# Performance work log

Hardware: AMD Instinct MI355X
Metric: run time of the kernel (lower is better)

The kernel has to match this reference:

```python
import jax, jax.numpy as jnp
import numpy as np

H, D, DIM = 8, 128, 1024   # heads, dim_head, model dim (inner_dim = H*D = DIM)
QB, N = 16, 512            # 'q' and 'n' dims of the [q, n, dim] inputs


def layer_norm(x, g, b, eps=1e-5):
    mu = x.mean(-1, keepdims=True)
    var = ((x - mu) ** 2).mean(-1, keepdims=True)
    return (x - mu) / jnp.sqrt(var + eps) * g + b


def setup_inputs() -> dict:
    key = jax.random.key(0)
    ks = jax.random.split(key, 8)
    rn = lambda k, shape, s=1.0: jax.random.normal(k, shape, jnp.float32) * s
    return {
        'q': rn(ks[0], (QB, N, DIM)),
        'k': rn(ks[1], (QB, N, DIM)),
        'v': rn(ks[2], (QB, N, DIM)),
        'ln_g': jnp.ones(DIM, jnp.float32),
        'ln_b': jnp.zeros(DIM, jnp.float32),
        'w_in': rn(ks[3], (H * D, DIM), 0.02),          # Linear(dim -> inner_dim), no bias
        'wp_w1': rn(ks[4], (D, 2 * D), 0.05),           # weight_predictor Linear(2d -> d)
        'wp_b1': jnp.zeros(D, jnp.float32),
        'wp_ln_g': jnp.ones(D, jnp.float32),
        'wp_ln_b': jnp.zeros(D, jnp.float32),
        'wp_w2': rn(ks[5], (3, D), 0.05),               # Linear(d -> 3)
        'wp_b2': jnp.zeros(3, jnp.float32),
        'w_out': rn(ks[6], (DIM, H * D), 0.02),         # output Linear(inner_dim -> dim)
        'b_out': jnp.zeros(DIM, jnp.float32),
    }


def reference(q, k, v, ln_g, ln_b, w_in, wp_w1, wp_b1, wp_ln_g, wp_ln_b,
              wp_w2, wp_b2, w_out, b_out):
    def proj(t):
        x = layer_norm(t, ln_g, ln_b) @ w_in.T                 # [Q, N, H*D]
        Qd, Nd = t.shape[0], t.shape[1]
        return x.reshape(Qd, Nd, H, D).transpose(2, 0, 1, 3)   # [h, q, n, d]

    f_q, f_k, f_v = proj(q), proj(k), proj(v)

    # cosine similarity component
    dots = jnp.einsum('hqnd,hqmd->hqnm', f_q, f_k)
    qn = jnp.linalg.norm(f_q, axis=-1)                          # [h, q, n]
    kn = jnp.linalg.norm(f_k, axis=-1)                          # [h, q, m]
    cosine_sim = dots / (qn[..., :, None] * kn[..., None, :])

    q_centered = f_q - f_q.mean(-1, keepdims=True)

    # variance component (unbiased variance, clipped ratio vs target_var=1)
    q_var = jnp.var(f_q, axis=-1, ddof=1)
    k_var = jnp.var(f_k, axis=-1, ddof=1)
    q_ratio = 2.0 * jnp.minimum(q_var, 1.0) / (q_var + 1.0)
    k_ratio = 2.0 * jnp.minimum(k_var, 1.0) / (k_var + 1.0)
    var_component = jnp.einsum('hqn,hqm->hqnm', q_ratio, k_ratio)

    # decorrelation-scaled covariance component (overwrites the dead loop in the source)
    q_flat = q_centered.reshape(H, -1, D)                        # [h, q*n, d]
    feat_corr = jnp.einsum('hnd,hne->hde', q_flat, q_flat) / q_flat.shape[1]
    feat_corr = feat_corr * (1.0 - jnp.eye(D, dtype=feat_corr.dtype))
    decorr_score = jnp.linalg.norm(feat_corr, axis=(-2, -1)) / (D * D)
    decorr_scale = jnp.exp(-5.0 * decorr_score)[:, None, None, None]
    cov_component = cosine_sim * decorr_scale

    # dynamic per-head weight mixing
    q_global = f_q.mean(axis=(1, 2))                             # [h, d]
    k_global = f_k.mean(axis=(1, 2))
    feats = jnp.concatenate([q_global, k_global], axis=-1)       # [h, 2d]
    h1 = jnp.maximum(layer_norm(feats @ wp_w1.T + wp_b1, wp_ln_g, wp_ln_b), 0.0)
    weights = jax.nn.softmax(h1 @ wp_w2.T + wp_b2, axis=-1)      # [h, 3]
    cw = weights[:, 0][:, None, None, None]
    vw = weights[:, 1][:, None, None, None]
    ww = weights[:, 2][:, None, None, None]
    mixed = cw * cosine_sim + vw * cov_component + ww * var_component

    out = jnp.einsum('hqnm,hqmd->hqnd', mixed, f_v)
    out = out.transpose(1, 2, 0, 3).reshape(q.shape[0], q.shape[1], H * D)
    return out @ w_out.T + b_out
```

## Files before the change

kernel.cpp:

```cpp
#include <hip/hip_runtime.h>
#include <hip/hip_bf16.h>

typedef unsigned short u16;
typedef __attribute__((ext_vector_type(8))) short short8;
typedef __attribute__((ext_vector_type(4))) float floatx4;

#define H 8
#define D 128
#define DIM 1024
#define QB 16
#define NSEQ 512
#define R 8192

__device__ inline u16 f2b(float x) {
    union { float f; unsigned int u; } c{x};
    unsigned int lsb = (c.u >> 16) & 1;
    unsigned int r = c.u + 0x7fffu + lsb;
    return (u16)(r >> 16);
}
__device__ inline float b2f(u16 u) {
    union { unsigned int i; float f; } c;
    c.i = (unsigned int)u << 16;
    return c.f;
}

#define GLOAD_LDS16(gptr, lptr)                                                        \
    __builtin_amdgcn_global_load_lds(                                                  \
        (const __attribute__((address_space(1))) unsigned int*)(gptr),                 \
        (__attribute__((address_space(3))) unsigned int*)(lptr), 16, 0, 0)

__global__ __launch_bounds__(256) void prep(const float* __restrict__ q,
                                            const float* __restrict__ k,
                                            const float* __restrict__ v,
                                            const float* __restrict__ g,
                                            const float* __restrict__ b,
                                            u16* __restrict__ out,
                                            const float* __restrict__ w_in,
                                            const float* __restrict__ w_out,
                                            u16* __restrict__ w_in16,
                                            u16* __restrict__ w_out16) {
    const int bb = blockIdx.x;
    const int tid = threadIdx.x;
    if (bb < 2048) {
        const int n4each = DIM * DIM / 4;
        int i = bb * 256 + tid;
        const float* src; u16* dst; int j;
        if (i < n4each) { src = w_in;  dst = w_in16;  j = i; }
        else            { src = w_out; dst = w_out16; j = i - n4each; }
        float4 vv = *(const float4*)(src + (size_t)j * 4);
        ushort4 pk;
        pk.x = f2b(vv.x); pk.y = f2b(vv.y); pk.z = f2b(vv.z); pk.w = f2b(vv.w);
        *(ushort4*)(dst + (size_t)j * 4) = pk;
        return;
    }
    const int b2 = bb - 2048;
    const int y = b2 >> 13;
    const int r = b2 & 8191;
    const float* src = (y == 0) ? q : (y == 1) ? k : v;
    const int wv = tid >> 6, lane = tid & 63;
    const float* row = src + (size_t)r * DIM;
    float4 vv = *(const float4*)(row + tid * 4);
    float sum = vv.x + vv.y + vv.z + vv.w;
    float sq = vv.x * vv.x + vv.y * vv.y + vv.z * vv.z + vv.w * vv.w;
#pragma unroll
    for (int o = 32; o > 0; o >>= 1) {
        sum += __shfl_xor(sum, o);
        sq  += __shfl_xor(sq, o);
    }
    __shared__ float s1[4], s2[4];
    if (lane == 0) { s1[wv] = sum; s2[wv] = sq; }
    __syncthreads();
    sum = s1[0] + s1[1] + s1[2] + s1[3];
    sq  = s2[0] + s2[1] + s2[2] + s2[3];
    float mean = sum * (1.0f / DIM);
    float var = sq * (1.0f / DIM) - mean * mean;
    float rstd = rsqrtf(var + 1e-5f);
    float4 gv = *(const float4*)(g + tid * 4);
    float4 bv = *(const float4*)(b + tid * 4);
    ushort4 pk;
    pk.x = f2b((vv.x - mean) * rstd * gv.x + bv.x);
    pk.y = f2b((vv.y - mean) * rstd * gv.y + bv.y);
    pk.z = f2b((vv.z - mean) * rstd * gv.z + bv.z);
    pk.w = f2b((vv.w - mean) * rstd * gv.w + bv.w);
    *(ushort4*)(out + ((size_t)y * R + r) * DIM + tid * 4) = pk;
}

__global__ __launch_bounds__(256) void gemm_qkv(const u16* __restrict__ A,
                                                const u16* __restrict__ B,
                                                u16* __restrict__ qT,
                                                u16* __restrict__ fqb,
                                                u16* __restrict__ kTh,
                                                u16* __restrict__ vT,
                                                float* __restrict__ qn,
                                                float* __restrict__ qm,
                                                float* __restrict__ qr,
                                                float* __restrict__ kn,
                                                float* __restrict__ kr) {
    __shared__ __align__(16) u16 smem[19712];
    u16* As  = smem;
    u16* Bs  = smem + 4096;
    u16* As2 = smem + 8192;
    u16* Bs2 = smem + 12288;
    float* sred = (float*)(smem + 18432);
    float* invb = (float*)(smem + 19456);

    const int tid = threadIdx.x;
    const int bb = blockIdx.x;
    const int xcd = bb & 7, j0 = bb >> 3;
    const int h = j0 & 7;
    const int rowblk = xcd * 24 + (j0 >> 3);
    const int m0 = rowblk * 128, n0 = h * 128;
    const int seg = rowblk >> 6;
    const int lrb = (rowblk & 63) * 128;

    const int wave = tid >> 6, lane = tid & 63;
    const int wm = (wave >> 1) * 64, wn = (wave & 1) * 64;
    const int fr = lane & 15, kq = lane >> 4;
    const int srow = tid >> 2, scol = (tid & 3) * 8;

    floatx4 acc[4][4] = {};
    const size_t aOff0 = (size_t)(m0 + srow) * DIM + scol;
    const size_t aOff1 = (size_t)(m0 + 64 + srow) * DIM + scol;
    const size_t bOff0 = (size_t)(n0 + srow) * DIM + scol;
    const size_t bOff1 = (size_t)(n0 + 64 + srow) * DIM + scol;

    for (int kt = 0; kt < DIM; kt += 64) {
        GLOAD_LDS16(A + aOff0 + kt, As + tid * 8);
        GLOAD_LDS16(A + aOff1 + kt, As + (256 + tid) * 8);
        GLOAD_LDS16(B + bOff0 + kt, Bs + tid * 8);
        GLOAD_LDS16(B + bOff1 + kt, Bs + (256 + tid) * 8);
        GLOAD_LDS16(A + aOff0 + kt + 32, As2 + tid * 8);
        GLOAD_LDS16(A + aOff1 + kt + 32, As2 + (256 + tid) * 8);
        GLOAD_LDS16(B + bOff0 + kt + 32, Bs2 + tid * 8);
        GLOAD_LDS16(B + bOff1 + kt + 32, Bs2 + (256 + tid) * 8);
        __syncthreads();
        short8 xf[4], wf[4];
#pragma unroll
        for (int i = 0; i < 4; i++)
            xf[i] = *(const short8*)&As[(wm + i * 16 + fr) * 32 + kq * 8];
#pragma unroll
        for (int j = 0; j < 4; j++)
            wf[j] = *(const short8*)&Bs[(wn + j * 16 + fr) * 32 + kq * 8];
#pragma unroll
        for (int j = 0; j < 4; j++)
#pragma unroll
            for (int i = 0; i < 4; i++)
                acc[j][i] = __builtin_amdgcn_mfma_f32_16x16x32_bf16(wf[j], xf[i], acc[j][i], 0, 0, 0);
        short8 xg[4], wg[4];
#pragma unroll
        for (int i = 0; i < 4; i++)
            xg[i] = *(const short8*)&As2[(wm + i * 16 + fr) * 32 + kq * 8];
#pragma unroll
        for (int j = 0; j < 4; j++)
            wg[j] = *(const short8*)&Bs2[(wn + j * 16 + fr) * 32 + kq * 8];
#pragma unroll
        for (int j = 0; j < 4; j++)
#pragma unroll
            for (int i = 0; i < 4; i++)
                acc[j][i] = __builtin_amdgcn_mfma_f32_16x16x32_bf16(wg[j], xg[i], acc[j][i], 0, 0, 0);
        __syncthreads();
    }

    if (seg <= 1) {
        const int half = wn >> 6;
#pragma unroll
        for (int i = 0; i < 4; i++) {
            float s = 0.0f, qs = 0.0f;
#pragma unroll
            for (int j = 0; j < 4; j++)
#pragma unroll
                for (int rg = 0; rg < 4; rg++) {
                    float vv = acc[j][i][rg];
                    s += vv; qs += vv * vv;
                }
            s += __shfl_xor(s, 16); qs += __shfl_xor(qs, 16);
            s += __shfl_xor(s, 32); qs += __shfl_xor(qs, 32);
            if (kq == 0) {
                int rl = wm + i * 16 + fr;
                sred[rl * 4 + half * 2 + 0] = s;
                sred[rl * 4 + half * 2 + 1] = qs;
            }
        }
        __syncthreads();
        if (tid < 128) {
            float sum = sred[tid * 4 + 0] + sred[tid * 4 + 2];
            float sq  = sred[tid * 4 + 1] + sred[tid * 4 + 3];
            float nrm = sqrtf(sq);
            float var = (sq - sum * sum * (1.0f / D)) * (1.0f / (D - 1));
            float ratio = 2.0f * fminf(var, 1.0f) / (var + 1.0f);
            size_t idx = (size_t)h * R + lrb + tid;
            if (seg == 0) {
                qn[idx] = nrm; qm[idx] = sum * (1.0f / D); qr[idx] = ratio;
            } else {
                kn[idx] = nrm; kr[idx] = ratio;
                invb[tid] = 1.0f / nrm;
            }
        }
        __syncthreads();
    }

    u16* dstT = (seg == 0) ? qT : (seg == 1) ? kTh : vT;
#pragma unroll
    for (int i = 0; i < 4; i++) {
        const int rl = wm + i * 16 + fr;
        const float sc = (seg == 1) ? invb[rl] : 1.0f;
#pragma unroll
        for (int j = 0; j < 4; j++) {
#pragma unroll
            for (int rg = 0; rg < 4; rg++) {
                const int cl = wn + j * 16 + kq * 4 + rg;
                dstT[(size_t)(h * D + cl) * R + lrb + rl] = f2b(acc[j][i][rg] * sc);
            }
        }
    }

    if (seg == 0) {
        __syncthreads();
        u16* Tw = smem + wave * 4608;
#pragma unroll
        for (int i = 0; i < 4; i++)
#pragma unroll
            for (int j = 0; j < 4; j++) {
                ushort4 pk;
                pk.x = f2b(acc[j][i][0]); pk.y = f2b(acc[j][i][1]);
                pk.z = f2b(acc[j][i][2]); pk.w = f2b(acc[j][i][3]);
                *(ushort4*)&Tw[(i * 16 + fr) * 72 + j * 16 + kq * 4] = pk;
            }
        __syncthreads();
#pragma unroll
        for (int p = 0; p < 16; p++) {
            int rloc = p * 4 + kq;
            int c4 = fr * 4;
            ushort4 v = *(const ushort4*)&Tw[rloc * 72 + c4];
            *(ushort4*)&fqb[(size_t)(lrb + wm + rloc) * DIM + h * D + wn + c4] = v;
        }
    }
}

__global__ __launch_bounds__(256) void fanout(const u16* __restrict__ qT,
                                              const u16* __restrict__ kTh,
                                              const u16* __restrict__ vT,
                                              const float* __restrict__ qm,
                                              const float* __restrict__ kn,
                                              const float* __restrict__ kr,
                                              float* __restrict__ qg,
                                              float* __restrict__ kg,
                                              float* __restrict__ ubuf,
                                              float* __restrict__ s2,
                                              float* __restrict__ P,
                                              u16* __restrict__ Mt,
                                              float* __restrict__ sv) {
    __shared__ __align__(16) u16 sm[8832];
    u16* As = sm;
    u16* Bs = sm + 4096;
    float* wbuf  = (float*)(sm + 8192);
    float* svred = (float*)(sm + 8256);
    float* redS  = (float*)(sm + 8768);

    const int bb = blockIdx.x;
    const int tid = threadIdx.x;
    const int wave = tid >> 6, lane = tid & 63;
    const int wm = (wave >> 1) * 64, wn = (wave & 1) * 64;
    const int fr = lane & 15, kq = lane >> 4;
    const int srow = tid >> 2, scol = (tid & 3) * 8;

    if (bb < 128) {
        const int qi = bb & 15, h = bb >> 4;
        const int m0g = qi * 512;
        const size_t a0 = (size_t)(h * D + srow) * R + m0g + scol;
        const size_t a1 = (size_t)(h * D + 64 + srow) * R + m0g + scol;
        const int e_id = tid & 127, mb16 = (tid >> 7) * 16;
        float svacc = 0.0f;
        floatx4 acc[4][4] = {};
        for (int kt = 0; kt < 512; kt += 32) {
            GLOAD_LDS16(vT + a0 + kt, As + tid * 8);
            GLOAD_LDS16(vT + a1 + kt, As + (256 + tid) * 8);
            GLOAD_LDS16(kTh + a0 + kt, Bs + tid * 8);
            GLOAD_LDS16(kTh + a1 + kt, Bs + (256 + tid) * 8);
            if (tid < 32) wbuf[tid] = kr[(size_t)h * R + m0g + kt + tid];
            __syncthreads();
            short8 af[4], bf[4];
#pragma unroll
            for (int i = 0; i < 4; i++)
                af[i] = *(const short8*)&As[(wm + i * 16 + fr) * 32 + kq * 8];
#pragma unroll
            for (int j = 0; j < 4; j++)
                bf[j] = *(const short8*)&Bs[(wn + j * 16 + fr) * 32 + kq * 8];
#pragma unroll
            for (int i = 0; i < 4; i++)
#pragma unroll
                for (int j = 0; j < 4; j++)
                    acc[i][j] = __builtin_amdgcn_mfma_f32_16x16x32_bf16(af[i], bf[j], acc[i][j], 0, 0, 0);
            {
                short8 va = *(const short8*)&As[e_id * 32 + mb16];
                short8 vb = *(const short8*)&As[e_id * 32 + mb16 + 8];
#pragma unroll
                for (int jm = 0; jm < 8; jm++)
                    svacc += b2f((u16)va[jm]) * wbuf[mb16 + jm];
#pragma unroll
                for (int jm = 0; jm < 8; jm++)
                    svacc += b2f((u16)vb[jm]) * wbuf[mb16 + 8 + jm];
            }
            __syncthreads();
        }
        u16* mb = Mt + (size_t)(h * QB + qi) * D * D;
#pragma unroll
        for (int i = 0; i < 4; i++) {
            int er = wm + i * 16 + kq * 4;
#pragma unroll
            for (int j = 0; j < 4; j++) {
                int dc = wn + j * 16 + fr;
#pragma unroll
                for (int r = 0; r < 4; r++)
                    mb[(size_t)(er + r) * D + dc] = f2b(acc[i][j][r]);
            }
        }
        svred[tid] = svacc;
        __syncthreads();
        if (tid < 128)
            sv[(size_t)(h * QB + qi) * D + tid] = svred[tid] + svred[tid + 128];
    } else if (bb < 192) {
        const int t = bb - 128;
        const int c = t & 7, h = t >> 3;
        floatx4 acc[4][4] = {};
        const size_t a0 = (size_t)(h * D + srow) * R + c * 1024 + scol;
        const size_t a1 = (size_t)(h * D + 64 + srow) * R + c * 1024 + scol;
        for (int kt = 0; kt < 1024; kt += 32) {
            GLOAD_LDS16(qT + a0 + kt, As + tid * 8);
            GLOAD_LDS16(qT + a1 + kt, As + (256 + tid) * 8);
            __syncthreads();
            short8 af[4], bf[4];
#pragma unroll
            for (int i = 0; i < 4; i++)
                af[i] = *(const short8*)&As[(wm + i * 16 + fr) * 32 + kq * 8];
#pragma unroll
            for (int j = 0; j < 4; j++)
                bf[j] = *(const short8*)&As[(wn + j * 16 + fr) * 32 + kq * 8];
#pragma unroll
            for (int i = 0; i < 4; i++)
#pragma unroll
                for (int j = 0; j < 4; j++)
                    acc[i][j] = __builtin_amdgcn_mfma_f32_16x16x32_bf16(af[i], bf[j], acc[i][j], 0, 0, 0);
            __syncthreads();
        }
        float* base = P + (size_t)(h * 8 + c) * (D * D);
#pragma unroll
        for (int i = 0; i < 4; i++) {
            int dr = wm + i * 16 + kq * 4;
#pragma unroll
            for (int j = 0; j < 4; j++) {
                int ec = wn + j * 16 + fr;
                float4 f4;
                f4.x = acc[i][j][0]; f4.y = acc[i][j][1];
                f4.z = acc[i][j][2]; f4.w = acc[i][j][3];
                *(float4*)&base[(size_t)ec * D + dr] = f4;
            }
        }
    } else {
        const int t = bb - 192;
        const int dg = t & 15, h = (t >> 4) & 7, mode = t >> 7;
        const u16* fT = mode ? kTh : qT;
        const float* wvec = mode ? kn : qm;
        const int wv = tid >> 6;
        float (*red)[4] = (float(*)[4])redS;
        const float* wp = wvec + (size_t)h * R;
        for (int dd = 0; dd < 8; dd++) {
            int d = dg * 8 + dd;
            const u16* rowp = fT + (size_t)(h * D + d) * R;
            float s = 0.0f, su = 0.0f;
            for (int it = 0; it < 8; it++) {
                int r = it * 1024 + tid * 4;
                uint2 pv = *(const uint2*)(rowp + r);
                float4 w = *(const float4*)(wp + r);
                float v0 = b2f((u16)(pv.x & 0xffffu)), v1 = b2f((u16)(pv.x >> 16));
                float v2 = b2f((u16)(pv.y & 0xffffu)), v3 = b2f((u16)(pv.y >> 16));
                if (mode) s += v0 * w.x + v1 * w.y + v2 * w.z + v3 * w.w;
                else {
                    s += v0 + v1 + v2 + v3;
                    su += v0 * w.x + v1 * w.y + v2 * w.z + v3 * w.w;
                }
            }
#pragma unroll
            for (int o = 32; o > 0; o >>= 1) {
                s += __shfl_xor(s, o);
                su += __shfl_xor(su, o);
            }
            if ((tid & 63) == 0) { red[0][wv] = s; red[1][wv] = su; }
            __syncthreads();
            if (tid == 0) {
                float S  = red[0][0] + red[0][1] + red[0][2] + red[0][3];
                float SU = red[1][0] + red[1][1] + red[1][2] + red[1][3];
                if (mode) kg[h * D + d] = S * (1.0f / R);
                else { qg[h * D + d] = S * (1.0f / R); ubuf[h * D + d] = SU; }
            }
            __syncthreads();
        }
        if (!mode && dg == 0) {
            float tt = 0.0f;
            for (int it = 0; it < 8; it++) {
                float4 m4 = *(const float4*)(qm + (size_t)h * R + it * 1024 + tid * 4);
                tt += m4.x * m4.x + m4.y * m4.y + m4.z * m4.z + m4.w * m4.w;
            }
#pragma unroll
            for (int o = 32; o > 0; o >>= 1) tt += __shfl_xor(tt, o);
            if ((tid & 63) == 0) red[0][wv] = tt;
            __syncthreads();
            if (tid == 0) s2[h] = red[0][0] + red[0][1] + red[0][2] + red[0][3];
        }
    }
}

__global__ __launch_bounds__(256) void decorr_sum(const float* __restrict__ P,
                                                  const float* __restrict__ ubuf,
                                                  const float* __restrict__ s2b,
                                                  float* __restrict__ Spart) {
    int bx = blockIdx.x, h = blockIdx.y, tid = threadIdx.x;
    float s2h = s2b[h];
    float S = 0.0f;
    for (int t = 0; t < 2; t++) {
        int de = bx * 512 + t * 256 + tid;
        int dd = de >> 7, ee = de & 127;
        float g = 0.0f;
        for (int c = 0; c < 8; c++)
            g += P[(size_t)(h * 8 + c) * (D * D) + de];
        if (dd != ee) {
            float vv = (g - ubuf[h * D + dd] - ubuf[h * D + ee] + s2h) * (1.0f / R);
            S += vv * vv;
        }
    }
#pragma unroll
    for (int o = 32; o > 0; o >>= 1) S += __shfl_xor(S, o);
    __shared__ float r1[4];
    if ((tid & 63) == 0) r1[tid >> 6] = S;
    __syncthreads();
    if (tid == 0) Spart[h * 32 + bx] = r1[0] + r1[1] + r1[2] + r1[3];
}

__global__ __launch_bounds__(256) void head_kernel(const float* __restrict__ Spart,
                                                   const float* __restrict__ qg,
                                                   const float* __restrict__ kg,
                                                   const float* __restrict__ w1,
                                                   const float* __restrict__ b1,
                                                   const float* __restrict__ lng,
                                                   const float* __restrict__ lnb,
                                                   const float* __restrict__ w2,
                                                   const float* __restrict__ b2,
                                                   float* __restrict__ coef) {
    int h = blockIdx.x, tid = threadIdx.x;
    __shared__ float s1[256], s2[256], s3[256];
    __shared__ float feats[256];
    float Ssum = 0.0f;
    for (int c = 0; c < 32; c++) Ssum += Spart[h * 32 + c];
    float dscale = expf(-5.0f * sqrtf(Ssum) / (float)(D * D));
    feats[tid] = (tid < 128) ? qg[h * D + tid] : kg[h * D + tid - 128];
    __syncthreads();
    float yv = 0.0f;
    if (tid < 128) {
        float a = b1[tid];
        for (int i = 0; i < 256; i++) a = fmaf(feats[i], w1[tid * 256 + i], a);
        yv = a;
    }
    s1[tid] = (tid < 128) ? yv : 0.0f;
    s2[tid] = (tid < 128) ? yv * yv : 0.0f;
    __syncthreads();
    for (int s = 128; s > 0; s >>= 1) {
        if (tid < s) { s1[tid] += s1[tid + s]; s2[tid] += s2[tid + s]; }
        __syncthreads();
    }
    float mean = s1[0] * (1.0f / 128.0f);
    float var = s2[0] * (1.0f / 128.0f) - mean * mean;
    float rstd = rsqrtf(var + 1e-5f);
    float rel = 0.0f;
    if (tid < 128)
        rel = fmaxf((yv - mean) * rstd * lng[tid] + lnb[tid], 0.0f);
    __syncthreads();
    s1[tid] = (tid < 128) ? rel * w2[0 * 128 + tid] : 0.0f;
    s2[tid] = (tid < 128) ? rel * w2[1 * 128 + tid] : 0.0f;
    s3[tid] = (tid < 128) ? rel * w2[2 * 128 + tid] : 0.0f;
    __syncthreads();
    for (int s = 128; s > 0; s >>= 1) {
        if (tid < s) { s1[tid] += s1[tid + s]; s2[tid] += s2[tid + s]; s3[tid] += s3[tid + s]; }
        __syncthreads();
    }
    if (tid == 0) {
        float g0 = s1[0] + b2[0], g1 = s2[0] + b2[1], g2 = s3[0] + b2[2];
        float mx = fmaxf(g0, fmaxf(g1, g2));
        float e0 = expf(g0 - mx), e1 = expf(g1 - mx), e2 = expf(g2 - mx);
        float inv = 1.0f / (e0 + e1 + e2);
        coef[h * 2 + 0] = e0 * inv + e1 * inv * dscale;
        coef[h * 2 + 1] = e2 * inv;
    }
}

__global__ __launch_bounds__(256) void attn_mfma(const u16* __restrict__ fqb,
                                                 const u16* __restrict__ Mt,
                                                 const float* __restrict__ qn,
                                                 const float* __restrict__ qr,
                                                 const float* __restrict__ sv,
                                                 const float* __restrict__ coef,
                                                 u16* __restrict__ outb) {
    __shared__ u16 As[128 * 32];
    __shared__ u16 Bs[128 * 32];
    const int nb = blockIdx.x, qi = blockIdx.y, h = blockIdx.z;
    const int tid = threadIdx.x;
    const int wave = tid >> 6, lane = tid & 63;
    const int wm = (wave >> 1) * 64, wn = (wave & 1) * 64;
    const int fr = lane & 15, kq = lane >> 4;
    const int srow = tid >> 2, scol = (tid & 3) * 8;
    const int n0g = qi * 512 + nb * 128;
    const size_t a0 = (size_t)(n0g + srow) * DIM + h * D + scol;
    const size_t a1 = (size_t)(n0g + 64 + srow) * DIM + h * D + scol;
    const u16* mtb = Mt + (size_t)(h * QB + qi) * D * D;
    floatx4 acc[4][4] = {};
    for (int kt = 0; kt < 128; kt += 32) {
        GLOAD_LDS16(fqb + a0 + kt, As + tid * 8);
        GLOAD_LDS16(fqb + a1 + kt, As + (256 + tid) * 8);
        GLOAD_LDS16(mtb + (size_t)srow * D + kt + scol, Bs + tid * 8);
        GLOAD_LDS16(mtb + (size_t)(64 + srow) * D + kt + scol, Bs + (256 + tid) * 8);
        __syncthreads();
        short8 af[4], bf[4];
#pragma unroll
        for (int i = 0; i < 4; i++)
            af[i] = *(const short8*)&As[(wm + i * 16 + fr) * 32 + kq * 8];
#pragma unroll
        for (int j = 0; j < 4; j++)
            bf[j] = *(const short8*)&Bs[(wn + j * 16 + fr) * 32 + kq * 8];
#pragma unroll
        for (int i = 0; i < 4; i++)
#pragma unroll
            for (int j = 0; j < 4; j++)
                acc[i][j] = __builtin_amdgcn_mfma_f32_16x16x32_bf16(af[i], bf[j], acc[i][j], 0, 0, 0);
        __syncthreads();
    }
    float c0 = coef[2 * h], c1 = coef[2 * h + 1];
#pragma unroll
    for (int i = 0; i < 4; i++) {
        int nr = n0g + wm + i * 16 + kq * 4;
        float4 nv = *(const float4*)&qn[(size_t)h * R + nr];
        float4 rv = *(const float4*)&qr[(size_t)h * R + nr];
        float sc1[4] = {c0 / nv.x, c0 / nv.y, c0 / nv.z, c0 / nv.w};
        float sc2[4] = {c1 * rv.x, c1 * rv.y, c1 * rv.z, c1 * rv.w};
#pragma unroll
        for (int j = 0; j < 4; j++) {
            int ec = wn + j * 16 + fr;
            float svv = sv[(size_t)(h * QB + qi) * D + ec];
#pragma unroll
            for (int r = 0; r < 4; r++)
                outb[(size_t)(nr + r) * DIM + h * D + ec] = f2b(sc1[r] * acc[i][j][r] + sc2[r] * svv);
        }
    }
}

__global__ __launch_bounds__(256) void gemm_out(const u16* __restrict__ A,
                                                const u16* __restrict__ B,
                                                const float* __restrict__ bias,
                                                float* __restrict__ C) {
    __shared__ u16 As[128 * 64];
    __shared__ u16 Bs[128 * 64];
    const int tid = threadIdx.x;
    const int bb = blockIdx.x;
    const int xcd = bb & 7, jj = bb >> 3;
    const int col = jj & 7, rowblk = xcd * 8 + (jj >> 3);
    const int m0 = rowblk * 128, n0 = col * 128;
    const int wave = tid >> 6, lane = tid & 63;
    const int wm = (wave >> 1) * 64, wn = (wave & 1) * 64;
    const int fr = lane & 15, kq = lane >> 4;
    const int srow = tid >> 2, scol = (tid & 3) * 8;
    floatx4 acc[4][4] = {};
    const size_t aOff0 = (size_t)(m0 + srow) * DIM + scol;
    const size_t aOff1 = (size_t)(m0 + 64 + srow) * DIM + scol;
    const size_t bOff0 = (size_t)(n0 + srow) * DIM + scol;
    const size_t bOff1 = (size_t)(n0 + 64 + srow) * DIM + scol;
    for (int kt = 0; kt < DIM; kt += 64) {
        GLOAD_LDS16(A + aOff0 + kt, As + tid * 8);
        GLOAD_LDS16(A + aOff1 + kt, As + (256 + tid) * 8);
        GLOAD_LDS16(A + aOff0 + kt + 32, As + (512 + tid) * 8);
        GLOAD_LDS16(A + aOff1 + kt + 32, As + (768 + tid) * 8);
        GLOAD_LDS16(B + bOff0 + kt, Bs + tid * 8);
        GLOAD_LDS16(B + bOff1 + kt, Bs + (256 + tid) * 8);
        GLOAD_LDS16(B + bOff0 + kt + 32, Bs + (512 + tid) * 8);
        GLOAD_LDS16(B + bOff1 + kt + 32, Bs + (768 + tid) * 8);
        __syncthreads();
        short8 af[4], bf[4];
#pragma unroll
        for (int i = 0; i < 4; i++)
            af[i] = *(const short8*)&As[(wm + i * 16 + fr) * 32 + kq * 8];
#pragma unroll
        for (int j = 0; j < 4; j++)
            bf[j] = *(const short8*)&Bs[(wn + j * 16 + fr) * 32 + kq * 8];
#pragma unroll
        for (int i = 0; i < 4; i++)
#pragma unroll
            for (int j = 0; j < 4; j++)
                acc[i][j] = __builtin_amdgcn_mfma_f32_16x16x32_bf16(af[i], bf[j], acc[i][j], 0, 0, 0);
        short8 ag[4], bg[4];
#pragma unroll
        for (int i = 0; i < 4; i++)
            ag[i] = *(const short8*)&As[4096 + (wm + i * 16 + fr) * 32 + kq * 8];
#pragma unroll
        for (int j = 0; j < 4; j++)
            bg[j] = *(const short8*)&Bs[4096 + (wn + j * 16 + fr) * 32 + kq * 8];
#pragma unroll
        for (int i = 0; i < 4; i++)
#pragma unroll
            for (int j = 0; j < 4; j++)
                acc[i][j] = __builtin_amdgcn_mfma_f32_16x16x32_bf16(ag[i], bg[j], acc[i][j], 0, 0, 0);
        __syncthreads();
    }
#pragma unroll
    for (int i = 0; i < 4; i++) {
        int rbase = m0 + wm + i * 16 + kq * 4;
#pragma unroll
        for (int j = 0; j < 4; j++) {
            int c = n0 + wn + j * 16 + fr;
            float badd = bias[c];
#pragma unroll
            for (int r = 0; r < 4; r++)
                C[(size_t)(rbase + r) * DIM + c] = acc[i][j][r] + badd;
        }
    }
}

extern "C" void kernel_launch(void* const* d_in, const int* in_sizes, int n_in,
                              void* d_out, int out_size, void* d_ws, size_t ws_size,
                              hipStream_t stream) {
    (void)in_sizes; (void)n_in; (void)out_size; (void)ws_size;
    const float* q      = (const float*)d_in[0];
    const float* k      = (const float*)d_in[1];
    const float* v      = (const float*)d_in[2];
    const float* ln_g   = (const float*)d_in[3];
    const float* ln_b   = (const float*)d_in[4];
    const float* w_in   = (const float*)d_in[5];
    const float* wp_w1  = (const float*)d_in[6];
    const float* wp_b1  = (const float*)d_in[7];
    const float* wp_lng = (const float*)d_in[8];
    const float* wp_lnb = (const float*)d_in[9];
    const float* wp_w2  = (const float*)d_in[10];
    const float* wp_b2  = (const float*)d_in[11];
    const float* w_out  = (const float*)d_in[12];
    const float* b_out  = (const float*)d_in[13];
    float* out = (float*)d_out;

    constexpr size_t F = (size_t)R * DIM;
    u16* lnall   = (u16*)d_ws;
    u16* fqb     = lnall + 3 * F;
    u16* qT      = fqb + F;
    u16* kTh     = qT + F;
    u16* vT      = kTh + F;
    u16* w_in16  = vT + F;
    u16* w_out16 = w_in16 + (size_t)DIM * DIM;
    u16* Mt      = w_out16 + (size_t)DIM * DIM;
    float* P     = (float*)(Mt + (size_t)H * QB * D * D);
    float* qn    = P + (size_t)32 * H * D * D;
    float* qm    = qn + (size_t)H * R;
    float* qr    = qm + (size_t)H * R;
    float* kn    = qr + (size_t)H * R;
    float* kr    = kn + (size_t)H * R;
    float* qg    = kr + (size_t)H * R;
    float* kg    = qg + H * D;
    float* ubuf  = kg + H * D;
    float* s2    = ubuf + H * D;
    float* Spart = s2 + H;
    float* coef  = Spart + H * 8;
    float* svb   = coef + 16;
    float* SpartN = qm;

    prep<<<26624, 256, 0, stream>>>(q, k, v, ln_g, ln_b, lnall,
                                    w_in, w_out, w_in16, w_out16);

    gemm_qkv<<<1536, 256, 0, stream>>>(lnall, w_in16, qT, fqb, kTh, vT,
                                       qn, qm, qr, kn, kr);

    fanout<<<448, 256, 0, stream>>>(qT, kTh, vT, qm, kn, kr,
                                    qg, kg, ubuf, s2, P, Mt, svb);

    decorr_sum<<<dim3(32, H), 256, 0, stream>>>(P, ubuf, s2, SpartN);

    head_kernel<<<H, 256, 0, stream>>>(SpartN, qg, kg, wp_w1, wp_b1,
                                       wp_lng, wp_lnb, wp_w2, wp_b2, coef);

    attn_mfma<<<dim3(4, QB, H), 256, 0, stream>>>(fqb, Mt, qn, qr, svb, coef, lnall);

    gemm_out<<<512, 256, 0, stream>>>(lnall, w_out16, b_out, out);
}
```

Measured before the change: 316.8 us.

## Use wave-per-row layernorm and deepen K-chunks per barrier in fanout/attn

The layernorm prep path now gives each wave one full row (four float4 loads per lane), which removes the shared-memory reduction and block barrier and cuts the prep grid from 26624 to 8192 blocks. The fanout kernel's two GEMM paths now stage two 32-wide K chunks per barrier pair, and attn_mfma loads the whole 128-deep K slice into LDS once with a single barrier. The aim is fewer barriers and more loads in flight per synchronisation, at the cost of larger LDS footprints that may reduce occupancy.

```diff
diff --git a/kernel.cpp b/kernel.cpp
--- a/kernel.cpp
+++ b/kernel.cpp
@@ -54,35 +54,43 @@
         return;
     }
     const int b2 = bb - 2048;
-    const int y = b2 >> 13;
-    const int r = b2 & 8191;
+    const int wv = tid >> 6, lane = tid & 63;
+    const int row = b2 * 4 + wv;
+    const int y = row >> 13, r = row & 8191;
     const float* src = (y == 0) ? q : (y == 1) ? k : v;
-    const int wv = tid >> 6, lane = tid & 63;
-    const float* row = src + (size_t)r * DIM;
-    float4 vv = *(const float4*)(row + tid * 4);
-    float sum = vv.x + vv.y + vv.z + vv.w;
-    float sq = vv.x * vv.x + vv.y * vv.y + vv.z * vv.z + vv.w * vv.w;
+    const float* rp = src + (size_t)r * DIM;
+    float4 x0 = *(const float4*)(rp + (0 * 64 + lane) * 4);
+    float4 x1 = *(const float4*)(rp + (1 * 64 + lane) * 4);
+    float4 x2 = *(const float4*)(rp + (2 * 64 + lane) * 4);
+    float4 x3 = *(const float4*)(rp + (3 * 64 + lane) * 4);
+    float sum = (x0.x + x0.y + x0.z + x0.w) + (x1.x + x1.y + x1.z + x1.w)
+              + (x2.x + x2.y + x2.z + x2.w) + (x3.x + x3.y + x3.z + x3.w);
+    float sq = x0.x*x0.x + x0.y*x0.y + x0.z*x0.z + x0.w*x0.w
+             + x1.x*x1.x + x1.y*x1.y + x1.z*x1.z + x1.w*x1.w
+             + x2.x*x2.x + x2.y*x2.y + x2.z*x2.z + x2.w*x2.w
+             + x3.x*x3.x + x3.y*x3.y + x3.z*x3.z + x3.w*x3.w;
 #pragma unroll
     for (int o = 32; o > 0; o >>= 1) {
         sum += __shfl_xor(sum, o);
         sq  += __shfl_xor(sq, o);
     }
-    __shared__ float s1[4], s2[4];
-    if (lane == 0) { s1[wv] = sum; s2[wv] = sq; }
-    __syncthreads();
-    sum = s1[0] + s1[1] + s1[2] + s1[3];
-    sq  = s2[0] + s2[1] + s2[2] + s2[3];
     float mean = sum * (1.0f / DIM);
     float var = sq * (1.0f / DIM) - mean * mean;
     float rstd = rsqrtf(var + 1e-5f);
-    float4 gv = *(const float4*)(g + tid * 4);
-    float4 bv = *(const float4*)(b + tid * 4);
-    ushort4 pk;
-    pk.x = f2b((vv.x - mean) * rstd * gv.x + bv.x);
-    pk.y = f2b((vv.y - mean) * rstd * gv.y + bv.y);
-    pk.z = f2b((vv.z - mean) * rstd * gv.z + bv.z);
-    pk.w = f2b((vv.w - mean) * rstd * gv.w + bv.w);
-    *(ushort4*)(out + ((size_t)y * R + r) * DIM + tid * 4) = pk;
+    u16* op = out + ((size_t)y * R + r) * DIM;
+    float4 xs[4] = {x0, x1, x2, x3};
+#pragma unroll
+    for (int p = 0; p < 4; p++) {
+        int e4 = (p * 64 + lane) * 4;
+        float4 gv = *(const float4*)(g + e4);
+        float4 bv = *(const float4*)(b + e4);
+        ushort4 pk;
+        pk.x = f2b((xs[p].x - mean) * rstd * gv.x + bv.x);
+        pk.y = f2b((xs[p].y - mean) * rstd * gv.y + bv.y);
+        pk.z = f2b((xs[p].z - mean) * rstd * gv.z + bv.z);
+        pk.w = f2b((xs[p].w - mean) * rstd * gv.w + bv.w);
+        *(ushort4*)(op + e4) = pk;
+    }
 }
 
 __global__ __launch_bounds__(256) void gemm_qkv(const u16* __restrict__ A,
@@ -250,12 +258,12 @@
                                               float* __restrict__ P,
                                               u16* __restrict__ Mt,
                                               float* __restrict__ sv) {
-    __shared__ __align__(16) u16 sm[8832];
+    __shared__ __align__(16) u16 sm[17040];
     u16* As = sm;
-    u16* Bs = sm + 4096;
-    float* wbuf  = (float*)(sm + 8192);
-    float* svred = (float*)(sm + 8256);
-    float* redS  = (float*)(sm + 8768);
+    u16* Bs = sm + 8192;
+    float* wbuf  = (float*)(sm + 16384);
+    float* svred = (float*)(sm + 16512);
+    float* redS  = (float*)(sm + 17024);
 
     const int bb = blockIdx.x;
     const int tid = threadIdx.x;
@@ -272,34 +280,38 @@
         const int e_id = tid & 127, mb16 = (tid >> 7) * 16;
         float svacc = 0.0f;
         floatx4 acc[4][4] = {};
-        for (int kt = 0; kt < 512; kt += 32) {
-            GLOAD_LDS16(vT + a0 + kt, As + tid * 8);
-            GLOAD_LDS16(vT + a1 + kt, As + (256 + tid) * 8);
-            GLOAD_LDS16(kTh + a0 + kt, Bs + tid * 8);
-            GLOAD_LDS16(kTh + a1 + kt, Bs + (256 + tid) * 8);
-            if (tid < 32) wbuf[tid] = kr[(size_t)h * R + m0g + kt + tid];
+        for (int kt = 0; kt < 512; kt += 64) {
+#pragma unroll
+            for (int kc = 0; kc < 2; kc++) {
+                GLOAD_LDS16(vT + a0 + kt + kc * 32, As + kc * 4096 + tid * 8);
+                GLOAD_LDS16(vT + a1 + kt + kc * 32, As + kc * 4096 + (256 + tid) * 8);
+                GLOAD_LDS16(kTh + a0 + kt + kc * 32, Bs + kc * 4096 + tid * 8);
+                GLOAD_LDS16(kTh + a1 + kt + kc * 32, Bs + kc * 4096 + (256 + tid) * 8);
+            }
+            if (tid < 64) wbuf[tid] = kr[(size_t)h * R + m0g + kt + tid];
             __syncthreads();
-            short8 af[4], bf[4];
-#pragma unroll
-            for (int i = 0; i < 4; i++)
-                af[i] = *(const short8*)&As[(wm + i * 16 + fr) * 32 + kq * 8];
-#pragma unroll
-            for (int j = 0; j < 4; j++)
-                bf[j] = *(const short8*)&Bs[(wn + j * 16 + fr) * 32 + kq * 8];
-#pragma unroll
-            for (int i = 0; i < 4; i++)
+#pragma unroll
+            for (int kc = 0; kc < 2; kc++) {
+                short8 af[4], bf[4];
+#pragma unroll
+                for (int i = 0; i < 4; i++)
+                    af[i] = *(const short8*)&As[kc * 4096 + (wm + i * 16 + fr) * 32 + kq * 8];
 #pragma unroll
                 for (int j = 0; j < 4; j++)
-                    acc[i][j] = __builtin_amdgcn_mfma_f32_16x16x32_bf16(af[i], bf[j], acc[i][j], 0, 0, 0);
-            {
-                short8 va = *(const short8*)&As[e_id * 32 + mb16];
-                short8 vb = *(const short8*)&As[e_id * 32 + mb16 + 8];
+                    bf[j] = *(const short8*)&Bs[kc * 4096 + (wn + j * 16 + fr) * 32 + kq * 8];
+#pragma unroll
+                for (int i = 0; i < 4; i++)
+#pragma unroll
+                    for (int j = 0; j < 4; j++)
+                        acc[i][j] = __builtin_amdgcn_mfma_f32_16x16x32_bf16(af[i], bf[j], acc[i][j], 0, 0, 0);
+                short8 va = *(const short8*)&As[kc * 4096 + e_id * 32 + mb16];
+                short8 vb = *(const short8*)&As[kc * 4096 + e_id * 32 + mb16 + 8];
 #pragma unroll
                 for (int jm = 0; jm < 8; jm++)
-                    svacc += b2f((u16)va[jm]) * wbuf[mb16 + jm];
+                    svacc += b2f((u16)va[jm]) * wbuf[kc * 32 + mb16 + jm];
 #pragma unroll
                 for (int jm = 0; jm < 8; jm++)
-                    svacc += b2f((u16)vb[jm]) * wbuf[mb16 + 8 + jm];
+                    svacc += b2f((u16)vb[jm]) * wbuf[kc * 32 + mb16 + 8 + jm];
             }
             __syncthreads();
         }
@@ -325,22 +337,28 @@
         floatx4 acc[4][4] = {};
         const size_t a0 = (size_t)(h * D + srow) * R + c * 1024 + scol;
         const size_t a1 = (size_t)(h * D + 64 + srow) * R + c * 1024 + scol;
-        for (int kt = 0; kt < 1024; kt += 32) {
-            GLOAD_LDS16(qT + a0 + kt, As + tid * 8);
-            GLOAD_LDS16(qT + a1 + kt, As + (256 + tid) * 8);
+        for (int kt = 0; kt < 1024; kt += 64) {
+#pragma unroll
+            for (int kc = 0; kc < 2; kc++) {
+                GLOAD_LDS16(qT + a0 + kt + kc * 32, As + kc * 4096 + tid * 8);
+                GLOAD_LDS16(qT + a1 + kt + kc * 32, As + kc * 4096 + (256 + tid) * 8);
+            }
             __syncthreads();
-            short8 af[4], bf[4];
-#pragma unroll
-            for (int i = 0; i < 4; i++)
-                af[i] = *(const short8*)&As[(wm + i * 16 + fr) * 32 + kq * 8];
-#pragma unroll
-            for (int j = 0; j < 4; j++)
-                bf[j] = *(const short8*)&As[(wn + j * 16 + fr) * 32 + kq * 8];
-#pragma unroll
-            for (int i = 0; i < 4; i++)
+#pragma unroll
+            for (int kc = 0; kc < 2; kc++) {
+                short8 af[4], bf[4];
+#pragma unroll
+                for (int i = 0; i < 4; i++)
+                    af[i] = *(const short8*)&As[kc * 4096 + (wm + i * 16 + fr) * 32 + kq * 8];
 #pragma unroll
                 for (int j = 0; j < 4; j++)
-                    acc[i][j] = __builtin_amdgcn_mfma_f32_16x16x32_bf16(af[i], bf[j], acc[i][j], 0, 0, 0);
+                    bf[j] = *(const short8*)&As[kc * 4096 + (wn + j * 16 + fr) * 32 + kq * 8];
+#pragma unroll
+                for (int i = 0; i < 4; i++)
+#pragma unroll
+                    for (int j = 0; j < 4; j++)
+                        acc[i][j] = __builtin_amdgcn_mfma_f32_16x16x32_bf16(af[i], bf[j], acc[i][j], 0, 0, 0);
+            }
             __syncthreads();
         }
         float* base = P + (size_t)(h * 8 + c) * (D * D);
@@ -499,8 +517,8 @@
                                                  const float* __restrict__ sv,
                                                  const float* __restrict__ coef,
                                                  u16* __restrict__ outb) {
-    __shared__ u16 As[128 * 32];
-    __shared__ u16 Bs[128 * 32];
+    __shared__ u16 As[128 * 128];
+    __shared__ u16 Bs[128 * 128];
     const int nb = blockIdx.x, qi = blockIdx.y, h = blockIdx.z;
     const int tid = threadIdx.x;
     const int wave = tid >> 6, lane = tid & 63;
@@ -511,26 +529,29 @@
     const size_t a0 = (size_t)(n0g + srow) * DIM + h * D + scol;
     const size_t a1 = (size_t)(n0g + 64 + srow) * DIM + h * D + scol;
     const u16* mtb = Mt + (size_t)(h * QB + qi) * D * D;
+#pragma unroll
+    for (int kc = 0; kc < 4; kc++) {
+        GLOAD_LDS16(fqb + a0 + kc * 32, As + kc * 4096 + tid * 8);
+        GLOAD_LDS16(fqb + a1 + kc * 32, As + kc * 4096 + (256 + tid) * 8);
+        GLOAD_LDS16(mtb + (size_t)srow * D + kc * 32 + scol, Bs + kc * 4096 + tid * 8);
+        GLOAD_LDS16(mtb + (size_t)(64 + srow) * D + kc * 32 + scol, Bs + kc * 4096 + (256 + tid) * 8);
+    }
+    __syncthreads();
     floatx4 acc[4][4] = {};
-    for (int kt = 0; kt < 128; kt += 32) {
-        GLOAD_LDS16(fqb + a0 + kt, As + tid * 8);
-        GLOAD_LDS16(fqb + a1 + kt, As + (256 + tid) * 8);
-        GLOAD_LDS16(mtb + (size_t)srow * D + kt + scol, Bs + tid * 8);
-        GLOAD_LDS16(mtb + (size_t)(64 + srow) * D + kt + scol, Bs + (256 + tid) * 8);
-        __syncthreads();
+#pragma unroll
+    for (int kc = 0; kc < 4; kc++) {
         short8 af[4], bf[4];
 #pragma unroll
         for (int i = 0; i < 4; i++)
-            af[i] = *(const short8*)&As[(wm + i * 16 + fr) * 32 + kq * 8];
+            af[i] = *(const short8*)&As[kc * 4096 + (wm + i * 16 + fr) * 32 + kq * 8];
 #pragma unroll
         for (int j = 0; j < 4; j++)
-            bf[j] = *(const short8*)&Bs[(wn + j * 16 + fr) * 32 + kq * 8];
+            bf[j] = *(const short8*)&Bs[kc * 4096 + (wn + j * 16 + fr) * 32 + kq * 8];
 #pragma unroll
         for (int i = 0; i < 4; i++)
 #pragma unroll
             for (int j = 0; j < 4; j++)
                 acc[i][j] = __builtin_amdgcn_mfma_f32_16x16x32_bf16(af[i], bf[j], acc[i][j], 0, 0, 0);
-        __syncthreads();
     }
     float c0 = coef[2 * h], c1 = coef[2 * h + 1];
 #pragma unroll
@@ -665,8 +686,8 @@
     float* svb   = coef + 16;
     float* SpartN = qm;
 
-    prep<<<26624, 256, 0, stream>>>(q, k, v, ln_g, ln_b, lnall,
-                                    w_in, w_out, w_in16, w_out16);
+    prep<<<8192, 256, 0, stream>>>(q, k, v, ln_g, ln_b, lnall,
+                                   w_in, w_out, w_in16, w_out16);
 
     gemm_qkv<<<1536, 256, 0, stream>>>(lnall, w_in16, qT, fqb, kTh, vT,
                                        qn, qm, qr, kn, kr);
```

Measured after the change: 314.0 us. About the same (-0.9%).
